# Kernel optimization log

Hardware: AMD Instinct MI355X
Metric: run time of the kernel (lower is better)

The kernel has to match this reference:

```python
import jax, jax.numpy as jnp
import numpy as np

D, H, E = 1024, 4096, 8


def setup_inputs() -> dict:
    key = jax.random.key(0)
    ks = jax.random.split(key, 8)
    s_in = 1.0 / np.sqrt(D)
    s_hid = 1.0 / np.sqrt(H)
    return {
        "x": jax.random.normal(ks[0], (4, 2048, D), dtype=jnp.float32),
        # torch nn.Linear init ~ U(-1/sqrt(fan_in), 1/sqrt(fan_in)); exact dist irrelevant for a numeric reference
        "Wg": jax.random.uniform(ks[1], (D, E), jnp.float32, -s_in, s_in),
        "bg": jax.random.uniform(ks[2], (E,), jnp.float32, -s_in, s_in),
        "W1": jax.random.uniform(ks[3], (E, D, H), jnp.float32, -s_in, s_in),
        "b1": jax.random.uniform(ks[4], (E, H), jnp.float32, -s_in, s_in),
        "W2": jax.random.uniform(ks[5], (E, H, D), jnp.float32, -s_hid, s_hid),
        "b2": jax.random.uniform(ks[6], (E, D), jnp.float32, -s_hid, s_hid),
    }


def reference(x, Wg, bg, W1, b1, W2, b2):
    # gate
    gate_logits = jnp.einsum("bsd,de->bse", x, Wg) + bg
    gate_probs = jax.nn.softmax(gate_logits, axis=-1)
    expert_indices = jnp.argmax(gate_probs, axis=-1)  # [B,S]

    # Faithful to source: mask the INPUT per expert, run the full MLP on the
    # masked input (biases still apply to zeroed tokens!), and sum all experts.
    onehot = jax.nn.one_hot(expert_indices, E, dtype=x.dtype)  # [B,S,E]
    xm = jnp.einsum("bsd,bse->ebsd", x, onehot)                # [E,B,S,D]
    h = jax.nn.relu(jnp.einsum("ebsd,edh->ebsh", xm, W1) + b1[:, None, None, :])
    out_e = jnp.einsum("ebsh,ehd->ebsd", h, W2) + b2[:, None, None, :]
    combined_output = jnp.sum(out_e, axis=0)                   # [B,S,D]
    return combined_output, gate_probs, expert_indices
```

## Files before the change

kernel.cpp:

```cpp
#include <hip/hip_runtime.h>
#include <hip/hip_bf16.h>
#include <cstdint>

#define D_DIM 1024
#define H_DIM 4096
#define E_NUM 8
#define NTOK  8192

#define BM 128
#define BN 128
#define BK 32

#define MAXT 72
#define NBY1 (H_DIM / BN)
#define NBY2 (D_DIM / BN)

typedef __bf16 bf16;
typedef __bf16 bf16x8 __attribute__((ext_vector_type(8)));
typedef __bf16 bf16x4 __attribute__((ext_vector_type(4)));
typedef float  f32x4  __attribute__((ext_vector_type(4)));

#define GLOAD16(g, l)                                                          \
    __builtin_amdgcn_global_load_lds(                                          \
        (const __attribute__((address_space(1))) void*)(g),                    \
        (__attribute__((address_space(3))) void*)(l), 16, 0, 0)

__global__ __launch_bounds__(256) void zero_kernel(int* cnt, float* cpartial)
{
    const int i = blockIdx.x * 256 + threadIdx.x;
    if (i < E_NUM * D_DIM) cpartial[i] = 0.f;
    if (i < E_NUM) cnt[i] = 0;
}

__global__ __launch_bounds__(256) void fused_aux_kernel(
    const float* __restrict__ W2, const float* __restrict__ W1,
    const float* __restrict__ b1,
    const float* __restrict__ x, const float* __restrict__ Wg,
    const float* __restrict__ bg,
    bf16* __restrict__ W2t, bf16* __restrict__ W1t,
    float* __restrict__ cpartial,
    float* __restrict__ out_probs, float* __restrict__ out_idx,
    int* __restrict__ cnt, int* __restrict__ list)
{
    __shared__ float T[64][65];
    const int b = blockIdx.x;
    const int t = threadIdx.x;

    if (b < 8192) {
        const int kx = b & 63, ny = (b >> 6) & 15, e = b >> 10;
        const int k0 = kx * 64, n0 = ny * 64;
        const float* src = W2 + (size_t)e * H_DIM * D_DIM;
        bf16* dst = W2t + (size_t)e * H_DIM * D_DIM;
        {
            const int ty = t >> 4, tx = (t & 15) * 4;
#pragma unroll
            for (int i = 0; i < 4; i++) {
                f32x4 v = __builtin_nontemporal_load(
                    (const f32x4*)(src + (size_t)(k0 + ty + 16 * i) * D_DIM + n0 + tx));
                T[ty + 16 * i][tx + 0] = v[0]; T[ty + 16 * i][tx + 1] = v[1];
                T[ty + 16 * i][tx + 2] = v[2]; T[ty + 16 * i][tx + 3] = v[3];
            }
        }
        __syncthreads();
        {
            const int n = t >> 2, kk = (t & 3) * 16;
            bf16 tmp[16];
#pragma unroll
            for (int j = 0; j < 16; j++) tmp[j] = (bf16)T[kk + j][n];
            *(bf16x8*)(dst + (size_t)(n0 + n) * H_DIM + k0 + kk)     = *(bf16x8*)&tmp[0];
            *(bf16x8*)(dst + (size_t)(n0 + n) * H_DIM + k0 + kk + 8) = *(bf16x8*)&tmp[8];
        }
        if (t < 64) {
            float s = 0.f;
#pragma unroll 8
            for (int h = 0; h < 64; h++)
                s += fmaxf(b1[(size_t)e * H_DIM + k0 + h], 0.f) * T[h][t];
            atomicAdd(&cpartial[(size_t)e * D_DIM + n0 + t], s);
        }
    } else if (b < 16384) {
        const int i2 = b - 8192;
        const int kx = i2 & 15, ny = (i2 >> 4) & 63, e = i2 >> 10;
        const int k0 = kx * 64, n0 = ny * 64;
        const float* src = W1 + (size_t)e * D_DIM * H_DIM;
        bf16* dst = W1t + (size_t)e * D_DIM * H_DIM;
        {
            const int ty = t >> 4, tx = (t & 15) * 4;
#pragma unroll
            for (int i = 0; i < 4; i++) {
                f32x4 v = __builtin_nontemporal_load(
                    (const f32x4*)(src + (size_t)(k0 + ty + 16 * i) * H_DIM + n0 + tx));
                T[ty + 16 * i][tx + 0] = v[0]; T[ty + 16 * i][tx + 1] = v[1];
                T[ty + 16 * i][tx + 2] = v[2]; T[ty + 16 * i][tx + 3] = v[3];
            }
        }
        __syncthreads();
        {
            const int n = t >> 2, kk = (t & 3) * 16;
            bf16 tmp[16];
#pragma unroll
            for (int j = 0; j < 16; j++) tmp[j] = (bf16)T[kk + j][n];
            *(bf16x8*)(dst + (size_t)(n0 + n) * D_DIM + k0 + kk)     = *(bf16x8*)&tmp[0];
            *(bf16x8*)(dst + (size_t)(n0 + n) * D_DIM + k0 + kk + 8) = *(bf16x8*)&tmp[8];
        }
    } else {
        const int tok = (b - 16384) * 4 + (t >> 6);
        const int l = t & 63;
        double part[E_NUM];
#pragma unroll
        for (int e = 0; e < E_NUM; e++) part[e] = 0.0;
        const float* xr = x + (size_t)tok * D_DIM;
#pragma unroll
        for (int i = 0; i < D_DIM / 64; i++) {
            const int d = l + i * 64;
            const float xv = xr[d];
            const float* wr = Wg + (size_t)d * E_NUM;
            float4 w0 = *(const float4*)(wr);
            float4 w1 = *(const float4*)(wr + 4);
            part[0] += (double)xv * (double)w0.x;
            part[1] += (double)xv * (double)w0.y;
            part[2] += (double)xv * (double)w0.z;
            part[3] += (double)xv * (double)w0.w;
            part[4] += (double)xv * (double)w1.x;
            part[5] += (double)xv * (double)w1.y;
            part[6] += (double)xv * (double)w1.z;
            part[7] += (double)xv * (double)w1.w;
        }
#pragma unroll
        for (int e = 0; e < E_NUM; e++) {
            double v = part[e];
            for (int s = 32; s > 0; s >>= 1) v += __shfl_xor(v, s, 64);
            part[e] = v;
        }
        if (l == 0) {
            float logits[E_NUM], probs[E_NUM];
            float m = -3.0e38f;
#pragma unroll
            for (int e = 0; e < E_NUM; e++) {
                logits[e] = (float)(part[e] + (double)bg[e]);
                m = fmaxf(m, logits[e]);
            }
            float s = 0.f;
#pragma unroll
            for (int e = 0; e < E_NUM; e++) { probs[e] = expf(logits[e] - m); s += probs[e]; }
            const float inv = 1.f / s;
            int best = 0; float bp = -1.f;
#pragma unroll
            for (int e = 0; e < E_NUM; e++) {
                probs[e] *= inv;
                if (probs[e] > bp) { bp = probs[e]; best = e; }
            }
#pragma unroll
            for (int e = 0; e < E_NUM; e++) out_probs[(size_t)tok * E_NUM + e] = probs[e];
            out_idx[tok] = (float)best;
            const int pos = atomicAdd(&cnt[best], 1);
            list[best * NTOK + pos] = tok;
        }
    }
}

__global__ void offsets_kernel(const int* __restrict__ cnt, int* __restrict__ off,
                               int* __restrict__ tile_e, int* __restrict__ tile_row,
                               int* __restrict__ tile_n)
{
    if (threadIdx.x == 0) {
        int a = 0, n = 0;
        for (int e = 0; e < E_NUM; e++) {
            off[e] = a; a += cnt[e];
            for (int rr = 0; rr < cnt[e]; rr += BM) {
                tile_e[n] = e; tile_row[n] = rr; n++;
            }
        }
        tile_n[0] = n;
    }
}

__global__ __launch_bounds__(256) void gather_kernel(
    const float* __restrict__ x, const int* __restrict__ off,
    const int* __restrict__ cnt, const int* __restrict__ list,
    bf16* __restrict__ Xg)
{
    const int p = blockIdx.x;
    int e = 0;
    while (e < E_NUM - 1 && p >= off[e] + cnt[e]) e++;
    const int token = list[e * NTOK + (p - off[e])];
    const float* src = x + (size_t)token * D_DIM;
    bf16* dst = Xg + (size_t)p * D_DIM;
    const int t = threadIdx.x;
    float4 v = *(const float4*)(src + t * 4);
    bf16x4 o;
    o[0] = (bf16)v.x; o[1] = (bf16)v.y; o[2] = (bf16)v.z; o[3] = (bf16)v.w;
    *(bf16x4*)(dst + t * 4) = o;
}

__global__ __launch_bounds__(256) void cfinal_kernel(
    const float* __restrict__ cpartial, const float* __restrict__ b2,
    float* __restrict__ adj)
{
    const int d = blockIdx.x * 256 + threadIdx.x;
    float c[E_NUM];
    float tot = 0.f;
#pragma unroll
    for (int e = 0; e < E_NUM; e++) {
        c[e] = cpartial[(size_t)e * D_DIM + d] + b2[(size_t)e * D_DIM + d];
        tot += c[e];
    }
#pragma unroll
    for (int e = 0; e < E_NUM; e++) adj[(size_t)e * D_DIM + d] = tot - c[e];
}

__global__ __launch_bounds__(256) void gemm1_kernel(
    const bf16* __restrict__ Xg, const bf16* __restrict__ W1t,
    const float* __restrict__ b1, const int* __restrict__ cnt,
    const int* __restrict__ off, const int* __restrict__ tile_e,
    const int* __restrict__ tile_row, const int* __restrict__ tile_n,
    bf16* __restrict__ Hb)
{
    const int orig = blockIdx.x;
    const int q = (MAXT * NBY1) >> 3;
    const int fid = (orig & 7) * q + (orig >> 3);
    const int tx = fid % MAXT;
    const int by = fid / MAXT;
    if (tx >= tile_n[0]) return;
    const int e  = tile_e[tx];
    const int m0 = tile_row[tx];
    const int ne = cnt[e];
    const int oe = off[e];

    __shared__ bf16 As[BM * BK];
    __shared__ bf16 Bs[BN * BK];

    const int t = threadIdx.x;
    const int w = t >> 6, lane = t & 63;
    const int wr = w >> 1, wc = w & 1;
    const int lrow = lane & 15, kq = (lane >> 4) * 8;

    const int lr = lane >> 2;
    const int lc = (lane & 3) * 8;
    const bf16* Ast = Xg + ((size_t)(oe + m0 + w * 32 + lr)) * D_DIM + lc;
    const bf16* Bst = W1t + ((size_t)e * H_DIM + by * BN + w * 32 + lr) * D_DIM + lc;
    bf16* Alds = As + (w * 32) * BK;
    bf16* Blds = Bs + (w * 32) * BK;

    f32x4 acc[4][4];
#pragma unroll
    for (int m = 0; m < 4; m++)
#pragma unroll
        for (int n = 0; n < 4; n++) acc[m][n] = (f32x4){0.f, 0.f, 0.f, 0.f};

    for (int kt = 0; kt < D_DIM / BK; kt++) {
        const int kc = kt * BK;
        GLOAD16(Ast + kc,              Alds);
        GLOAD16(Ast + 16 * D_DIM + kc, Alds + 16 * BK);
        GLOAD16(Bst + kc,              Blds);
        GLOAD16(Bst + 16 * D_DIM + kc, Blds + 16 * BK);
        __syncthreads();

        bf16x8 af[4], bfr[4];
#pragma unroll
        for (int m = 0; m < 4; m++)
            af[m] = *(const bf16x8*)&As[(wr * 64 + m * 16 + lrow) * BK + kq];
#pragma unroll
        for (int n = 0; n < 4; n++)
            bfr[n] = *(const bf16x8*)&Bs[(wc * 64 + n * 16 + lrow) * BK + kq];
#pragma unroll
        for (int m = 0; m < 4; m++)
#pragma unroll
            for (int n = 0; n < 4; n++)
                acc[m][n] = __builtin_amdgcn_mfma_f32_16x16x32_bf16(af[m], bfr[n], acc[m][n], 0, 0, 0);
        __syncthreads();
    }

#pragma unroll
    for (int m = 0; m < 4; m++) {
        const int rb0 = m0 + wr * 64 + m * 16 + ((lane >> 4) << 2);
#pragma unroll
        for (int n = 0; n < 4; n++) {
            const int gcol = by * BN + wc * 64 + n * 16 + (lane & 15);
            const float bias = b1[(size_t)e * H_DIM + gcol];
#pragma unroll
            for (int r = 0; r < 4; r++) {
                const int grow = rb0 + r;
                if (grow < ne) {
                    float v = acc[m][n][r] + bias;
                    Hb[((size_t)(oe + grow)) * H_DIM + gcol] = (bf16)fmaxf(v, 0.f);
                }
            }
        }
    }
}

__global__ __launch_bounds__(256) void gemm2_kernel(
    const bf16* __restrict__ Hb, const bf16* __restrict__ W2t,
    const float* __restrict__ b2, const float* __restrict__ adj,
    const int* __restrict__ cnt, const int* __restrict__ off,
    const int* __restrict__ tile_e, const int* __restrict__ tile_row,
    const int* __restrict__ tile_n, const int* __restrict__ list,
    float* __restrict__ out)
{
    const int orig = blockIdx.x;
    const int q = (MAXT * NBY2) >> 3;
    const int fid = (orig & 7) * q + (orig >> 3);
    const int tx = fid % MAXT;
    const int by = fid / MAXT;
    if (tx >= tile_n[0]) return;
    const int e  = tile_e[tx];
    const int m0 = tile_row[tx];
    const int ne = cnt[e];
    const int oe = off[e];

    __shared__ bf16 As[BM * BK];
    __shared__ bf16 Bs[BN * BK];

    const int t = threadIdx.x;
    const int w = t >> 6, lane = t & 63;
    const int wr = w >> 1, wc = w & 1;
    const int lrow = lane & 15, kq = (lane >> 4) * 8;

    const int lr = lane >> 2;
    const int lc = (lane & 3) * 8;
    const bf16* Ast = Hb + ((size_t)(oe + m0 + w * 32 + lr)) * H_DIM + lc;
    const bf16* Bst = W2t + ((size_t)e * D_DIM + by * BN + w * 32 + lr) * H_DIM + lc;
    bf16* Alds = As + (w * 32) * BK;
    bf16* Blds = Bs + (w * 32) * BK;

    f32x4 acc[4][4];
#pragma unroll
    for (int m = 0; m < 4; m++)
#pragma unroll
        for (int n = 0; n < 4; n++) acc[m][n] = (f32x4){0.f, 0.f, 0.f, 0.f};

    for (int kt = 0; kt < H_DIM / BK; kt++) {
        const int kc = kt * BK;
        GLOAD16(Ast + kc,              Alds);
        GLOAD16(Ast + 16 * H_DIM + kc, Alds + 16 * BK);
        GLOAD16(Bst + kc,              Blds);
        GLOAD16(Bst + 16 * H_DIM + kc, Blds + 16 * BK);
        __syncthreads();

        bf16x8 af[4], bfr[4];
#pragma unroll
        for (int m = 0; m < 4; m++)
            af[m] = *(const bf16x8*)&As[(wr * 64 + m * 16 + lrow) * BK + kq];
#pragma unroll
        for (int n = 0; n < 4; n++)
            bfr[n] = *(const bf16x8*)&Bs[(wc * 64 + n * 16 + lrow) * BK + kq];
#pragma unroll
        for (int m = 0; m < 4; m++)
#pragma unroll
            for (int n = 0; n < 4; n++)
                acc[m][n] = __builtin_amdgcn_mfma_f32_16x16x32_bf16(af[m], bfr[n], acc[m][n], 0, 0, 0);
        __syncthreads();
    }

#pragma unroll
    for (int m = 0; m < 4; m++) {
        const int rb0 = m0 + wr * 64 + m * 16 + ((lane >> 4) << 2);
#pragma unroll
        for (int n = 0; n < 4; n++) {
            const int gcol = by * BN + wc * 64 + n * 16 + (lane & 15);
            const float badj = b2[(size_t)e * D_DIM + gcol] + adj[(size_t)e * D_DIM + gcol];
#pragma unroll
            for (int r = 0; r < 4; r++) {
                const int grow = rb0 + r;
                if (grow < ne) {
                    const int tok = list[e * NTOK + grow];
                    out[(size_t)tok * D_DIM + gcol] = acc[m][n][r] + badj;
                }
            }
        }
    }
}

extern "C" void kernel_launch(void* const* d_in, const int* in_sizes, int n_in,
                              void* d_out, int out_size, void* d_ws, size_t ws_size,
                              hipStream_t stream)
{
    (void)in_sizes; (void)n_in; (void)out_size; (void)ws_size;
    const float* x  = (const float*)d_in[0];
    const float* Wg = (const float*)d_in[1];
    const float* bg = (const float*)d_in[2];
    const float* W1 = (const float*)d_in[3];
    const float* b1 = (const float*)d_in[4];
    const float* W2 = (const float*)d_in[5];
    const float* b2 = (const float*)d_in[6];

    float* out_comb  = (float*)d_out;
    float* out_probs = out_comb + (size_t)NTOK * D_DIM;
    float* out_idx   = out_probs + (size_t)NTOK * E_NUM;

    char* ws = (char*)d_ws;
    size_t o = 0;
    bf16* W1t = (bf16*)(ws + o); o += (size_t)E_NUM * H_DIM * D_DIM * 2;
    bf16* W2t = (bf16*)(ws + o); o += (size_t)E_NUM * H_DIM * D_DIM * 2;
    bf16* Hb  = (bf16*)(ws + o); o += (size_t)NTOK * H_DIM * 2;
    bf16* Xg  = (bf16*)(ws + o); o += (size_t)NTOK * D_DIM * 2;
    float* cpartial = (float*)(ws + o); o += (size_t)E_NUM * D_DIM * 4;
    float* adj      = (float*)(ws + o); o += (size_t)E_NUM * D_DIM * 4;
    int* cnt  = (int*)(ws + o); o += 256;
    int* off  = (int*)(ws + o); o += 256;
    int* tile_e   = (int*)(ws + o); o += 512;
    int* tile_row = (int*)(ws + o); o += 512;
    int* tile_n   = (int*)(ws + o); o += 256;
    int* list = (int*)(ws + o); o += (size_t)E_NUM * NTOK * 4;

    zero_kernel<<<(E_NUM * D_DIM + 255) / 256, 256, 0, stream>>>(cnt, cpartial);
    fused_aux_kernel<<<18432, 256, 0, stream>>>(W2, W1, b1, x, Wg, bg,
                                                W2t, W1t, cpartial,
                                                out_probs, out_idx, cnt, list);
    offsets_kernel<<<1, 64, 0, stream>>>(cnt, off, tile_e, tile_row, tile_n);
    gather_kernel<<<NTOK, 256, 0, stream>>>(x, off, cnt, list, Xg);
    cfinal_kernel<<<D_DIM / 256, 256, 0, stream>>>(cpartial, b2, adj);
    gemm1_kernel<<<MAXT * NBY1, 256, 0, stream>>>(Xg, W1t, b1, cnt, off, tile_e, tile_row, tile_n, Hb);
    gemm2_kernel<<<MAXT * NBY2, 256, 0, stream>>>(Hb, W2t, b2, adj, cnt, off, tile_e, tile_row, tile_n, list, out_comb);
}
```

Baseline: 425.6 us.

## Fuse W1 fp32-to-bf16 transpose into gemm1 B-tile loading

Drops the separate pass that converted and transposed W1 into a bf16 workspace copy, along with its 8192 blocks in the aux kernel. Instead, gemm1 reads fp32 W1 directly each K-step, converts it to bf16 in registers and writes it transposed into LDS. This removes a full write and re-read of the 64 MB bf16 W1 copy. In exchange, every gemm1 tile reloads fp32 weights (twice the bytes) across many row tiles per expert and loses the async global-to-LDS load for B. It also adds scattered 4-byte LDS stores that may cause bank conflicts.

```diff
diff --git a/kernel.cpp b/kernel.cpp
--- a/kernel.cpp
+++ b/kernel.cpp
@@ -18,6 +18,7 @@
 typedef __bf16 bf16;
 typedef __bf16 bf16x8 __attribute__((ext_vector_type(8)));
 typedef __bf16 bf16x4 __attribute__((ext_vector_type(4)));
+typedef __bf16 bf16x2 __attribute__((ext_vector_type(2)));
 typedef float  f32x4  __attribute__((ext_vector_type(4)));
 
 #define GLOAD16(g, l)                                                          \
@@ -33,12 +34,10 @@
 }
 
 __global__ __launch_bounds__(256) void fused_aux_kernel(
-    const float* __restrict__ W2, const float* __restrict__ W1,
-    const float* __restrict__ b1,
+    const float* __restrict__ W2, const float* __restrict__ b1,
     const float* __restrict__ x, const float* __restrict__ Wg,
     const float* __restrict__ bg,
-    bf16* __restrict__ W2t, bf16* __restrict__ W1t,
-    float* __restrict__ cpartial,
+    bf16* __restrict__ W2t, float* __restrict__ cpartial,
     float* __restrict__ out_probs, float* __restrict__ out_idx,
     int* __restrict__ cnt, int* __restrict__ list)
 {
@@ -77,33 +76,8 @@
                 s += fmaxf(b1[(size_t)e * H_DIM + k0 + h], 0.f) * T[h][t];
             atomicAdd(&cpartial[(size_t)e * D_DIM + n0 + t], s);
         }
-    } else if (b < 16384) {
-        const int i2 = b - 8192;
-        const int kx = i2 & 15, ny = (i2 >> 4) & 63, e = i2 >> 10;
-        const int k0 = kx * 64, n0 = ny * 64;
-        const float* src = W1 + (size_t)e * D_DIM * H_DIM;
-        bf16* dst = W1t + (size_t)e * D_DIM * H_DIM;
-        {
-            const int ty = t >> 4, tx = (t & 15) * 4;
-#pragma unroll
-            for (int i = 0; i < 4; i++) {
-                f32x4 v = __builtin_nontemporal_load(
-                    (const f32x4*)(src + (size_t)(k0 + ty + 16 * i) * H_DIM + n0 + tx));
-                T[ty + 16 * i][tx + 0] = v[0]; T[ty + 16 * i][tx + 1] = v[1];
-                T[ty + 16 * i][tx + 2] = v[2]; T[ty + 16 * i][tx + 3] = v[3];
-            }
-        }
-        __syncthreads();
-        {
-            const int n = t >> 2, kk = (t & 3) * 16;
-            bf16 tmp[16];
-#pragma unroll
-            for (int j = 0; j < 16; j++) tmp[j] = (bf16)T[kk + j][n];
-            *(bf16x8*)(dst + (size_t)(n0 + n) * D_DIM + k0 + kk)     = *(bf16x8*)&tmp[0];
-            *(bf16x8*)(dst + (size_t)(n0 + n) * D_DIM + k0 + kk + 8) = *(bf16x8*)&tmp[8];
-        }
     } else {
-        const int tok = (b - 16384) * 4 + (t >> 6);
+        const int tok = (b - 8192) * 4 + (t >> 6);
         const int l = t & 63;
         double part[E_NUM];
 #pragma unroll
@@ -209,7 +183,7 @@
 }
 
 __global__ __launch_bounds__(256) void gemm1_kernel(
-    const bf16* __restrict__ Xg, const bf16* __restrict__ W1t,
+    const bf16* __restrict__ Xg, const float* __restrict__ W1,
     const float* __restrict__ b1, const int* __restrict__ cnt,
     const int* __restrict__ off, const int* __restrict__ tile_e,
     const int* __restrict__ tile_row, const int* __restrict__ tile_n,
@@ -237,9 +211,12 @@
     const int lr = lane >> 2;
     const int lc = (lane & 3) * 8;
     const bf16* Ast = Xg + ((size_t)(oe + m0 + w * 32 + lr)) * D_DIM + lc;
-    const bf16* Bst = W1t + ((size_t)e * H_DIM + by * BN + w * 32 + lr) * D_DIM + lc;
     bf16* Alds = As + (w * 32) * BK;
-    bf16* Blds = Bs + (w * 32) * BK;
+
+    const int bg = t & 15;
+    const int bk = (t >> 4) * 2;
+    const float* Bsrc = W1 + (size_t)e * D_DIM * H_DIM
+                      + (size_t)bk * H_DIM + by * BN + bg * 8;
 
     f32x4 acc[4][4];
 #pragma unroll
@@ -249,10 +226,20 @@
 
     for (int kt = 0; kt < D_DIM / BK; kt++) {
         const int kc = kt * BK;
+        const float* bp = Bsrc + (size_t)kc * H_DIM;
+        float4 r0a = *(const float4*)(bp);
+        float4 r0b = *(const float4*)(bp + 4);
+        float4 r1a = *(const float4*)(bp + H_DIM);
+        float4 r1b = *(const float4*)(bp + H_DIM + 4);
         GLOAD16(Ast + kc,              Alds);
         GLOAD16(Ast + 16 * D_DIM + kc, Alds + 16 * BK);
-        GLOAD16(Bst + kc,              Blds);
-        GLOAD16(Bst + 16 * D_DIM + kc, Blds + 16 * BK);
+        float r0[8] = {r0a.x, r0a.y, r0a.z, r0a.w, r0b.x, r0b.y, r0b.z, r0b.w};
+        float r1[8] = {r1a.x, r1a.y, r1a.z, r1a.w, r1b.x, r1b.y, r1b.z, r1b.w};
+#pragma unroll
+        for (int c = 0; c < 8; c++) {
+            bf16x2 v; v[0] = (bf16)r0[c]; v[1] = (bf16)r1[c];
+            *(bf16x2*)&Bs[(bg * 8 + c) * BK + bk] = v;
+        }
         __syncthreads();
 
         bf16x8 af[4], bfr[4];
@@ -402,14 +389,15 @@
     int* tile_row = (int*)(ws + o); o += 512;
     int* tile_n   = (int*)(ws + o); o += 256;
     int* list = (int*)(ws + o); o += (size_t)E_NUM * NTOK * 4;
+    (void)W1t;
 
     zero_kernel<<<(E_NUM * D_DIM + 255) / 256, 256, 0, stream>>>(cnt, cpartial);
-    fused_aux_kernel<<<18432, 256, 0, stream>>>(W2, W1, b1, x, Wg, bg,
-                                                W2t, W1t, cpartial,
+    fused_aux_kernel<<<10240, 256, 0, stream>>>(W2, b1, x, Wg, bg,
+                                                W2t, cpartial,
                                                 out_probs, out_idx, cnt, list);
     offsets_kernel<<<1, 64, 0, stream>>>(cnt, off, tile_e, tile_row, tile_n);
     gather_kernel<<<NTOK, 256, 0, stream>>>(x, off, cnt, list, Xg);
     cfinal_kernel<<<D_DIM / 256, 256, 0, stream>>>(cpartial, b2, adj);
-    gemm1_kernel<<<MAXT * NBY1, 256, 0, stream>>>(Xg, W1t, b1, cnt, off, tile_e, tile_row, tile_n, Hb);
+    gemm1_kernel<<<MAXT * NBY1, 256, 0, stream>>>(Xg, W1, b1, cnt, off, tile_e, tile_row, tile_n, Hb);
     gemm2_kernel<<<MAXT * NBY2, 256, 0, stream>>>(Hb, W2t, b2, adj, cnt, off, tile_e, tile_row, tile_n, list, out_comb);
 }
```

After: 517.4 us. 21.6% more time.
